# Kernel tuning notes

Measured on AMD Instinct MI355X. Metric: run time of the kernel, lower is better.

## Reference

```python
import jax, jax.numpy as jnp
import numpy as np

EPS = 1e-12  # matches torch F.normalize eps

def _l2norm(x, axis):
    n = jnp.sqrt(jnp.sum(x * x, axis=axis, keepdims=True))
    return x / jnp.maximum(n, EPS)

def setup_inputs() -> dict:
    key = jax.random.key(0)
    k1, k2, k3, k4 = jax.random.split(key, 4)
    b, n_way, k_shot, q, c, h, w = 2, 5, 5, 75, 64, 21, 21
    return {
        "support_xf": jax.random.normal(k1, (b, n_way * k_shot, c, h, w), dtype=jnp.float32),
        "support_y": jax.random.randint(k2, (b, n_way * k_shot), 0, n_way),
        "query_xf": jax.random.normal(k3, (b, q, c, h, w), dtype=jnp.float32),
        "query_y": jax.random.randint(k4, (b, q), 0, n_way),
        "n_way": n_way,
        "k_shot": k_shot,
    }

def reference(support_xf, support_y, query_xf, query_y, n_way, k_shot):
    b, q, c, h, w = query_xf.shape
    hw = h * w
    # k_shot averaging: (b, n_way, k_shot, c, h, w) -> mean over shots -> (b, n_way, c, hw)
    sup = support_xf.reshape(b, n_way, k_shot, c, hw).mean(axis=2)
    qry = query_xf.reshape(b, q, c, hw)
    # cosine similarity: L2-normalize each local descriptor along channel dim
    sup_n = _l2norm(sup, axis=2)  # (b, n_way, c, hw_s)
    qry_n = _l2norm(qry, axis=2)  # (b, q, c, hw_q)
    # inner product matrix: (b, q, n_way, hw_q, hw_s)
    sim = jnp.einsum('bqcm,bwcn->bqwmn', qry_n, sup_n)
    # topk with k=1 along support descriptors, mean over k == max
    topv = jnp.max(sim, axis=-1)  # (b, q, n_way, hw_q)
    logits = topv.sum(axis=-1).reshape(b * q, n_way)  # image-to-class score
    return logits
```

## Files before the change

kernel.cpp:

```cpp
#include <hip/hip_runtime.h>
#include <hip/hip_bf16.h>

namespace {
constexpr int kB = 2, kW = 5, kS = 5, kQ = 75, kC = 64, kHW = 441;
constexpr int kNP = 448;
constexpr int kMP = 448;
constexpr int kNT = kNP / 32;
constexpr int kCHUNK = 112;
constexpr int kLDT = 65;

typedef short bf16x8 __attribute__((ext_vector_type(8)));
typedef float f32x16 __attribute__((ext_vector_type(16)));
}

__global__ __launch_bounds__(256) void prep_k(const float* __restrict__ sup,
                                              const float* __restrict__ qry,
                                              unsigned short* __restrict__ snT,
                                              unsigned short* __restrict__ qnT) {
  __shared__ float img_t[kCHUNK * kLDT];
  __shared__ float inv[kCHUNK];
  const int tid = threadIdx.x;
  const int blk = blockIdx.x;

  int m0, mcnt;
  unsigned short* dst;
  const bool is_sup = blk < kB * kW * 4;

  if (is_sup) {
    int bw = blk >> 2, chunk = blk & 3;
    m0 = chunk * kCHUNK;
    mcnt = min(kCHUNK, kHW - m0);
    const float* base = sup + (size_t)bw * kS * kC * kHW;
    for (int i = tid; i < kC * kCHUNK; i += 256) {
      int c = i / kCHUNK, mm = i % kCHUNK;
      float v = 0.f;
      if (mm < mcnt) {
        const float* p = base + (size_t)c * kHW + m0 + mm;
        float s = 0.f;
#pragma unroll
        for (int k = 0; k < kS; ++k) s += p[(size_t)k * kC * kHW];
        v = s * (1.f / kS);
      }
      img_t[mm * kLDT + c] = v;
    }
    dst = snT + (size_t)bw * kNP * kC;
  } else {
    int qb = blk - kB * kW * 4;
    int bq = qb >> 2, chunk = qb & 3;
    m0 = chunk * kCHUNK;
    mcnt = min(kCHUNK, kHW - m0);
    const float* base = qry + (size_t)bq * kC * kHW;
    for (int i = tid; i < kC * kCHUNK; i += 256) {
      int c = i / kCHUNK, mm = i % kCHUNK;
      img_t[mm * kLDT + c] = (mm < mcnt) ? base[(size_t)c * kHW + m0 + mm] : 0.f;
    }
    dst = qnT + (size_t)bq * kMP * kC;
  }
  __syncthreads();

  if (tid < kCHUNK) {
    float ss = 0.f;
#pragma unroll
    for (int c = 0; c < kC; ++c) { float v = img_t[tid * kLDT + c]; ss += v * v; }
    inv[tid] = 1.f / fmaxf(sqrtf(ss), 1e-12f);
  }
  __syncthreads();

  for (int i8 = tid; i8 < kCHUNK * 8; i8 += 256) {
    int m = i8 >> 3, c8 = (i8 & 7) * 8;
    float sc = inv[m];
    union { unsigned short u[8]; uint4 v; } pk;
#pragma unroll
    for (int j = 0; j < 8; ++j) {
      __hip_bfloat16 o = __float2bfloat16(img_t[m * kLDT + c8 + j] * sc);
      pk.u[j] = *reinterpret_cast<unsigned short*>(&o);
    }
    *reinterpret_cast<uint4*>(dst + ((size_t)(m0 + m) * kC + c8)) = pk.v;
  }
}

__device__ __forceinline__ float max16_v(const f32x16& a) {
  float m0 = fmaxf(fmaxf(a[0], a[1]), a[2]);
  float m1 = fmaxf(fmaxf(a[3], a[4]), a[5]);
  float m2 = fmaxf(fmaxf(a[6], a[7]), a[8]);
  float m3 = fmaxf(fmaxf(a[9], a[10]), a[11]);
  float m4 = fmaxf(fmaxf(a[12], a[13]), a[14]);
  float t0 = fmaxf(fmaxf(m0, m1), m2);
  float t1 = fmaxf(fmaxf(m3, m4), a[15]);
  return fmaxf(t0, t1);
}
__device__ __forceinline__ float max12_v(const f32x16& a) {
  float m0 = fmaxf(fmaxf(a[0], a[1]), a[2]);
  float m1 = fmaxf(fmaxf(a[3], a[4]), a[5]);
  float m2 = fmaxf(fmaxf(a[6], a[7]), a[8]);
  float m3 = fmaxf(fmaxf(a[9], a[10]), a[11]);
  return fmaxf(fmaxf(m0, m1), fmaxf(m2, m3));
}

__global__ __launch_bounds__(256) void dn4_main_k(const unsigned short* __restrict__ qnT,
                                                  const unsigned short* __restrict__ snT,
                                                  float* __restrict__ out) {
  __shared__ unsigned short As[kNP * kC];
  const int idx = blockIdx.x;
  const int w = idx % kW;
  const int bq = idx / kW;
  const int b = bq / kQ;
  const int tid = threadIdx.x;

  {
    const uint4* src = reinterpret_cast<const uint4*>(snT + (size_t)(b * kW + w) * kNP * kC);
    uint4* dst = reinterpret_cast<uint4*>(As);
#pragma unroll
    for (int it = 0; it < (kNP * kC / 8) / 256; ++it) {
      int i = it * 256 + tid;
      int n = i >> 3, k16 = i & 7;
      dst[n * 8 + (k16 ^ (n & 7))] = src[i];
    }
  }

  const int lane = tid & 63;
  const int half = lane >> 5;
  const int lm = lane & 31;
  const int wid = tid >> 6;
  const int ct0 = (wid < 2) ? wid * 4 : 8 + (wid - 2) * 3;
  const int nct = (wid < 2) ? 4 : 3;

  bf16x8 bf[4][4];
  const unsigned short* qb = qnT + (size_t)bq * kMP * kC;
#pragma unroll
  for (int ct = 0; ct < 4; ++ct) {
    if (ct < nct) {
      int m = (ct0 + ct) * 32 + lm;
#pragma unroll
      for (int kk = 0; kk < 4; ++kk)
        bf[ct][kk] = *reinterpret_cast<const bf16x8*>(qb + (size_t)m * kC + kk * 16 + half * 8);
    }
  }
  __syncthreads();

  f32x16 z;
#pragma unroll
  for (int r = 0; r < 16; ++r) z[r] = 0.f;
  float rm[4] = {-INFINITY, -INFINITY, -INFINITY, -INFINITY};

  for (int nt = 0; nt < kNT; ++nt) {
    bf16x8 af[4];
    int n = nt * 32 + lm;
#pragma unroll
    for (int kk = 0; kk < 4; ++kk) {
      int k16 = kk * 2 + half;
      af[kk] = *reinterpret_cast<const bf16x8*>(As + ((size_t)(n * 8 + (k16 ^ (n & 7))) << 3));
    }
    if (nt < kNT - 1) {
#pragma unroll
      for (int ct = 0; ct < 4; ++ct) {
        if (ct < nct) {
          f32x16 acc = z;
#pragma unroll
          for (int kk = 0; kk < 4; ++kk)
            acc = __builtin_amdgcn_mfma_f32_32x32x16_bf16(af[kk], bf[ct][kk], acc, 0, 0, 0);
          rm[ct] = fmaxf(rm[ct], max16_v(acc));
        }
      }
    } else {
#pragma unroll
      for (int ct = 0; ct < 4; ++ct) {
        if (ct < nct) {
          f32x16 acc = z;
#pragma unroll
          for (int kk = 0; kk < 4; ++kk)
            acc = __builtin_amdgcn_mfma_f32_32x32x16_bf16(af[kk], bf[ct][kk], acc, 0, 0, 0);
          float t = max12_v(acc);
          if (half == 0) t = fmaxf(t, acc[12]);
          rm[ct] = fmaxf(rm[ct], t);
        }
      }
    }
  }

  float s = 0.f;
#pragma unroll
  for (int ct = 0; ct < 4; ++ct) {
    if (ct < nct) s += fmaxf(rm[ct], __shfl_xor(rm[ct], 32, 64));
  }
#pragma unroll
  for (int off = 1; off < 32; off <<= 1) s += __shfl_xor(s, off, 64);

  __shared__ float part[4];
  if (lane == 0) part[wid] = s;
  __syncthreads();
  if (tid == 0) out[idx] = part[0] + part[1] + part[2] + part[3];
}

extern "C" void kernel_launch(void* const* d_in, const int* in_sizes, int n_in,
                              void* d_out, int out_size, void* d_ws, size_t ws_size,
                              hipStream_t stream) {
  const float* sup = (const float*)d_in[0];
  const float* qry = (const float*)d_in[2];
  float* out = (float*)d_out;

  unsigned short* snT = (unsigned short*)d_ws;
  unsigned short* qnT = snT + (size_t)kB * kW * kNP * kC;

  int prep_blocks = kB * kW * 4 + kB * kQ * 4;
  prep_k<<<prep_blocks, 256, 0, stream>>>(sup, qry, snT, qnT);
  dn4_main_k<<<kB * kQ * kW, 256, 0, stream>>>(qnT, snT, out);
}
```

Measured before the change: 44.52 us.

## Drop LDS staging of support tile, stream A from global with XCD-aware block mapping

The main kernel no longer copies the normalized support descriptors into shared memory. Each lane now loads A fragments straight from global/L2 with a two-stage software double buffer across n-tiles. Both kernels remap block indices so that consecutive tiles, which share support and query data, land on the same XCD, keeping reused rows in that XCD's L2. The prep grid is reshuffled to match that mapping. This removes the LDS fill, the barrier and the LDS bandwidth use, but relies on L2 hits and gives up some load coalescing.

Measured after the change: 53.08 us. +19.2%, slower.

```diff
diff --git a/kernel.cpp b/kernel.cpp
--- a/kernel.cpp
+++ b/kernel.cpp
@@ -5,9 +5,10 @@
 constexpr int kB = 2, kW = 5, kS = 5, kQ = 75, kC = 64, kHW = 441;
 constexpr int kNP = 448;
 constexpr int kMP = 448;
-constexpr int kNT = kNP / 32;
 constexpr int kCHUNK = 112;
 constexpr int kLDT = 65;
+constexpr int kTiles = kB * kQ * kW;
+constexpr int kPrepGrid = 8 * 81;
 
 typedef short bf16x8 __attribute__((ext_vector_type(8)));
 typedef float f32x16 __attribute__((ext_vector_type(16)));
@@ -20,16 +21,34 @@
   __shared__ float img_t[kCHUNK * kLDT];
   __shared__ float inv[kCHUNK];
   const int tid = threadIdx.x;
-  const int blk = blockIdx.x;
-
-  int m0, mcnt;
+  const int x = blockIdx.x & 7;
+  const int j = blockIdx.x >> 3;
+
+  const int start0 = (x < 6) ? 94 * x : 564 + 93 * (x - 6);
+  const int start1 = (x + 1 < 6) ? 94 * (x + 1) : 564 + 93 * (x + 1 - 6);
+  const int lo = (start0 + 4) / 5, hi = (start1 + 4) / 5;
+  const int nq = 4 * (hi - lo);
+
+  bool is_sup;
+  int bw = 0, bq = 0, chunk;
+  if (j < nq) {
+    is_sup = false;
+    bq = lo + (j >> 2);
+    chunk = j & 3;
+  } else {
+    int js = j - nq;
+    if (js >= 5) return;
+    is_sup = true;
+    int u = x + 8 * js;
+    bw = u >> 2;
+    chunk = u & 3;
+  }
+
+  const int m0 = chunk * kCHUNK;
+  const int mcnt = min(kCHUNK, kHW - m0);
   unsigned short* dst;
-  const bool is_sup = blk < kB * kW * 4;
 
   if (is_sup) {
-    int bw = blk >> 2, chunk = blk & 3;
-    m0 = chunk * kCHUNK;
-    mcnt = min(kCHUNK, kHW - m0);
     const float* base = sup + (size_t)bw * kS * kC * kHW;
     for (int i = tid; i < kC * kCHUNK; i += 256) {
       int c = i / kCHUNK, mm = i % kCHUNK;
@@ -45,10 +64,6 @@
     }
     dst = snT + (size_t)bw * kNP * kC;
   } else {
-    int qb = blk - kB * kW * 4;
-    int bq = qb >> 2, chunk = qb & 3;
-    m0 = chunk * kCHUNK;
-    mcnt = min(kCHUNK, kHW - m0);
     const float* base = qry + (size_t)bq * kC * kHW;
     for (int i = tid; i < kC * kCHUNK; i += 256) {
       int c = i / kCHUNK, mm = i % kCHUNK;
@@ -71,9 +86,9 @@
     float sc = inv[m];
     union { unsigned short u[8]; uint4 v; } pk;
 #pragma unroll
-    for (int j = 0; j < 8; ++j) {
-      __hip_bfloat16 o = __float2bfloat16(img_t[m * kLDT + c8 + j] * sc);
-      pk.u[j] = *reinterpret_cast<unsigned short*>(&o);
+    for (int jj = 0; jj < 8; ++jj) {
+      __hip_bfloat16 o = __float2bfloat16(img_t[m * kLDT + c8 + jj] * sc);
+      pk.u[jj] = *reinterpret_cast<unsigned short*>(&o);
     }
     *reinterpret_cast<uint4*>(dst + ((size_t)(m0 + m) * kC + c8)) = pk.v;
   }
@@ -85,9 +100,7 @@
   float m2 = fmaxf(fmaxf(a[6], a[7]), a[8]);
   float m3 = fmaxf(fmaxf(a[9], a[10]), a[11]);
   float m4 = fmaxf(fmaxf(a[12], a[13]), a[14]);
-  float t0 = fmaxf(fmaxf(m0, m1), m2);
-  float t1 = fmaxf(fmaxf(m3, m4), a[15]);
-  return fmaxf(t0, t1);
+  return fmaxf(fmaxf(fmaxf(m0, m1), m2), fmaxf(fmaxf(m3, m4), a[15]));
 }
 __device__ __forceinline__ float max12_v(const f32x16& a) {
   float m0 = fmaxf(fmaxf(a[0], a[1]), a[2]);
@@ -97,86 +110,89 @@
   return fmaxf(fmaxf(m0, m1), fmaxf(m2, m3));
 }
 
+__device__ __forceinline__ void ldA(bf16x8 af[4], const unsigned short* arow, int nt) {
+  const unsigned short* p = arow + (size_t)nt * 32 * kC;
+#pragma unroll
+  for (int kk = 0; kk < 4; ++kk)
+    af[kk] = *reinterpret_cast<const bf16x8*>(p + kk * 16);
+}
+
+template <bool TAIL>
+__device__ __forceinline__ void do_nt(const bf16x8 af[4], const bf16x8 bf[4][4],
+                                      int nct, int lh, float rm[4]) {
+  f32x16 z;
+#pragma unroll
+  for (int r = 0; r < 16; ++r) z[r] = 0.f;
+#pragma unroll
+  for (int ct = 0; ct < 4; ++ct) {
+    if (ct < nct) {
+      f32x16 acc = z;
+#pragma unroll
+      for (int kk = 0; kk < 4; ++kk)
+        acc = __builtin_amdgcn_mfma_f32_32x32x16_bf16(af[kk], bf[ct][kk], acc, 0, 0, 0);
+      if (!TAIL) {
+        rm[ct] = fmaxf(rm[ct], max16_v(acc));
+      } else {
+        float t = max12_v(acc);
+        if (lh == 0) t = fmaxf(t, acc[12]);
+        rm[ct] = fmaxf(rm[ct], t);
+      }
+    }
+  }
+}
+
 __global__ __launch_bounds__(256) void dn4_main_k(const unsigned short* __restrict__ qnT,
                                                   const unsigned short* __restrict__ snT,
                                                   float* __restrict__ out) {
-  __shared__ unsigned short As[kNP * kC];
-  const int idx = blockIdx.x;
+  __shared__ float part[4];
+  const int tid = threadIdx.x;
+
+  const int xcd = blockIdx.x & 7, jj = blockIdx.x >> 3;
+  const int idx = (xcd < 6) ? xcd * 94 + jj : 564 + (xcd - 6) * 93 + jj;
+
   const int w = idx % kW;
   const int bq = idx / kW;
   const int b = bq / kQ;
-  const int tid = threadIdx.x;
-
-  {
-    const uint4* src = reinterpret_cast<const uint4*>(snT + (size_t)(b * kW + w) * kNP * kC);
-    uint4* dst = reinterpret_cast<uint4*>(As);
-#pragma unroll
-    for (int it = 0; it < (kNP * kC / 8) / 256; ++it) {
-      int i = it * 256 + tid;
-      int n = i >> 3, k16 = i & 7;
-      dst[n * 8 + (k16 ^ (n & 7))] = src[i];
-    }
-  }
 
   const int lane = tid & 63;
-  const int half = lane >> 5;
+  const int lh = lane >> 5;
   const int lm = lane & 31;
   const int wid = tid >> 6;
   const int ct0 = (wid < 2) ? wid * 4 : 8 + (wid - 2) * 3;
   const int nct = (wid < 2) ? 4 : 3;
 
+  const unsigned short* sb = snT + (size_t)(b * kW + w) * kNP * kC;
+  const unsigned short* qb = qnT + (size_t)bq * kMP * kC;
+
   bf16x8 bf[4][4];
-  const unsigned short* qb = qnT + (size_t)bq * kMP * kC;
 #pragma unroll
   for (int ct = 0; ct < 4; ++ct) {
     if (ct < nct) {
       int m = (ct0 + ct) * 32 + lm;
 #pragma unroll
-      for (int kk = 0; kk < 4; ++kk)
-        bf[ct][kk] = *reinterpret_cast<const bf16x8*>(qb + (size_t)m * kC + kk * 16 + half * 8);
-    }
-  }
-  __syncthreads();
-
-  f32x16 z;
-#pragma unroll
-  for (int r = 0; r < 16; ++r) z[r] = 0.f;
+      for (int kk = 0; kk < 4; ++kk) {
+        bf[ct][kk] = *reinterpret_cast<const bf16x8*>(qb + (size_t)m * kC + kk * 16 + lh * 8);
+        asm volatile("" : "+v"(bf[ct][kk]));
+      }
+    }
+  }
+
+  const unsigned short* arow = sb + (size_t)lm * kC + lh * 8;
+
   float rm[4] = {-INFINITY, -INFINITY, -INFINITY, -INFINITY};
-
-  for (int nt = 0; nt < kNT; ++nt) {
-    bf16x8 af[4];
-    int n = nt * 32 + lm;
-#pragma unroll
-    for (int kk = 0; kk < 4; ++kk) {
-      int k16 = kk * 2 + half;
-      af[kk] = *reinterpret_cast<const bf16x8*>(As + ((size_t)(n * 8 + (k16 ^ (n & 7))) << 3));
-    }
-    if (nt < kNT - 1) {
-#pragma unroll
-      for (int ct = 0; ct < 4; ++ct) {
-        if (ct < nct) {
-          f32x16 acc = z;
-#pragma unroll
-          for (int kk = 0; kk < 4; ++kk)
-            acc = __builtin_amdgcn_mfma_f32_32x32x16_bf16(af[kk], bf[ct][kk], acc, 0, 0, 0);
-          rm[ct] = fmaxf(rm[ct], max16_v(acc));
-        }
-      }
-    } else {
-#pragma unroll
-      for (int ct = 0; ct < 4; ++ct) {
-        if (ct < nct) {
-          f32x16 acc = z;
-#pragma unroll
-          for (int kk = 0; kk < 4; ++kk)
-            acc = __builtin_amdgcn_mfma_f32_32x32x16_bf16(af[kk], bf[ct][kk], acc, 0, 0, 0);
-          float t = max12_v(acc);
-          if (half == 0) t = fmaxf(t, acc[12]);
-          rm[ct] = fmaxf(rm[ct], t);
-        }
-      }
-    }
-  }
+  bf16x8 a0[4], a1[4];
+  ldA(a0, arow, 0);
+
+#pragma unroll 1
+  for (int t = 0; t < 6; ++t) {
+    ldA(a1, arow, 2 * t + 1);
+    do_nt<false>(a0, bf, nct, lh, rm);
+    ldA(a0, arow, 2 * t + 2);
+    do_nt<false>(a1, bf, nct, lh, rm);
+  }
+  ldA(a1, arow, 13);
+  do_nt<false>(a0, bf, nct, lh, rm);
+  do_nt<true>(a1, bf, nct, lh, rm);
 
   float s = 0.f;
 #pragma unroll
@@ -186,7 +202,6 @@
 #pragma unroll
   for (int off = 1; off < 32; off <<= 1) s += __shfl_xor(s, off, 64);
 
-  __shared__ float part[4];
   if (lane == 0) part[wid] = s;
   __syncthreads();
   if (tid == 0) out[idx] = part[0] + part[1] + part[2] + part[3];
@@ -202,7 +217,6 @@
   unsigned short* snT = (unsigned short*)d_ws;
   unsigned short* qnT = snT + (size_t)kB * kW * kNP * kC;
 
-  int prep_blocks = kB * kW * 4 + kB * kQ * 4;
-  prep_k<<<prep_blocks, 256, 0, stream>>>(sup, qry, snT, qnT);
-  dn4_main_k<<<kB * kQ * kW, 256, 0, stream>>>(qnT, snT, out);
-}
+  prep_k<<<kPrepGrid, 256, 0, stream>>>(sup, qry, snT, qnT);
+  dn4_main_k<<<kTiles, 256, 0, stream>>>(qnT, snT, out);
+}
```
